# Kernel tuning notes

Hardware: AMD Instinct MI355X
Metric: run time of the kernel (lower is better)

## Reference

```python
import jax, jax.numpy as jnp
import numpy as np

H = 1024   # hidden_size
V = 32000  # output_size (vocab)
B = 64     # batch
S = 2048   # encoder seq_len


def setup_inputs() -> dict:
    key = jax.random.key(0)
    ks = jax.random.split(key, 12)
    sc = 0.02
    return {
        "input_seq": jax.random.randint(ks[0], (B,), 0, V),
        "last_hidden": jax.random.normal(ks[1], (1, B, H), jnp.float32),
        "encoder_outputs": jax.random.normal(ks[2], (S, B, H), jnp.float32),
        "emb": jax.random.normal(ks[3], (V, H), jnp.float32) * sc,
        "w_ih": jax.random.normal(ks[4], (3 * H, H), jnp.float32) * sc,
        "w_hh": jax.random.normal(ks[5], (3 * H, H), jnp.float32) * sc,
        "b_ih": jnp.zeros((3 * H,), jnp.float32),
        "b_hh": jnp.zeros((3 * H,), jnp.float32),
        "attn_w": jax.random.normal(ks[6], (H, H), jnp.float32) * sc,
        "attn_b": jnp.zeros((H,), jnp.float32),
        "concat_w": jax.random.normal(ks[7], (H, 2 * H), jnp.float32) * sc,
        "concat_b": jnp.zeros((H,), jnp.float32),
        "out_w": jax.random.normal(ks[8], (V, H), jnp.float32) * sc,
        "out_b": jnp.zeros((V,), jnp.float32),
    }


def _forward(input_seq, last_hidden, encoder_outputs, emb, w_ih, w_hh, b_ih, b_hh,
             attn_w, attn_b, concat_w, concat_b, out_w, out_b):
    # 1. embedding (dropout = identity in eval)
    x = emb[input_seq]                      # [b, h]
    h = last_hidden[0]                      # [b, h]
    # 2. single-step GRU (PyTorch gate order: reset, update, new)
    gx = x @ w_ih.T + b_ih                  # [b, 3h]
    gh = h @ w_hh.T + b_hh                  # [b, 3h]
    r = jax.nn.sigmoid(gx[:, :H] + gh[:, :H])
    z = jax.nn.sigmoid(gx[:, H:2 * H] + gh[:, H:2 * H])
    n = jnp.tanh(gx[:, 2 * H:] + r * gh[:, 2 * H:])
    h_new = (1.0 - z) * n + z * h           # [b, h] = rnn_output
    # 3. Luong 'general' attention: score = y . (W enc + b)
    proj = jnp.einsum('sbh,gh->sbg', encoder_outputs, attn_w) + attn_b  # [s,b,h]
    scores = jnp.einsum('bh,sbh->bs', h_new, proj)                      # [b,s]
    attn_weights = jax.nn.softmax(scores, axis=-1)                      # [b,s]
    # 4. context = weights bmm encoder_outputs
    context = jnp.einsum('bs,sbh->bh', attn_weights, encoder_outputs)   # [b,h]
    # 5. concat -> linear -> tanh -> out
    cat = jnp.concatenate([h_new, context], axis=-1)                    # [b,2h]
    concat_output = jnp.tanh(cat @ concat_w.T + concat_b)               # [b,h]
    output = concat_output @ out_w.T + out_b                            # [b,V]
    return output, h_new[None], attn_weights[:, None, :]


def reference(input_seq, last_hidden, encoder_outputs, emb, w_ih, w_hh, b_ih, b_hh,
              attn_w, attn_b, concat_w, concat_b, out_w, out_b):
    return _forward(input_seq, last_hidden, encoder_outputs, emb, w_ih, w_hh, b_ih,
                    b_hh, attn_w, attn_b, concat_w, concat_b, out_w, out_b)
```

## Files before the change

### kernel.cpp

```cpp
#include <hip/hip_runtime.h>

#define HS 1024
#define VS 32000
#define BS 64
#define SS 2048
#define NCH 128
#define SCH (SS/NCH)

typedef __attribute__((ext_vector_type(4))) float f4v;
typedef __attribute__((ext_vector_type(8))) short s8v;

__device__ __forceinline__ float sigmf(float x) { return 1.0f / (1.0f + __expf(-x)); }

__device__ __forceinline__ short bf16c(float f) {
  unsigned u = __builtin_bit_cast(unsigned, f);
  u = (u + 0x7FFFu + ((u >> 16) & 1u)) >> 16;
  return (short)u;
}

__global__ __launch_bounds__(256) void k_prep(const int* __restrict__ idx,
    const float* __restrict__ emb, const float* __restrict__ hid,
    const float* __restrict__ aw, float* __restrict__ ht,
    short* __restrict__ fx, short* __restrict__ fh, short* __restrict__ awf) {
  int t = blockIdx.x * 256 + threadIdx.x;
  {
    int lane = t & 63, nt = (t >> 6) & 63, kt = t >> 12;
    int kr = kt * 32 + ((lane >> 4) & 3) * 8;
    int col = nt * 16 + (lane & 15);
    const float* sp = aw + (size_t)kr * HS + col;
    s8v v;
#pragma unroll
    for (int j = 0; j < 8; j++) v[j] = bf16c(sp[(size_t)j * HS]);
    *(s8v*)(awf + (size_t)t * 8) = v;
  }
  if (t < 65536) {
    int b = t >> 10, k = t & 1023;
    ht[k * BS + b] = hid[(size_t)b * HS + k];
  }
  if (t < 8192) {
    int lane = t & 63, ct = (t >> 6) & 3, kt = t >> 8;
    int col = ct * 16 + (lane & 15);
    int kr = kt * 32 + ((lane >> 4) & 3) * 8;
    const float* sp = emb + (size_t)idx[col] * HS + kr;
    s8v v;
#pragma unroll
    for (int j = 0; j < 8; j++) v[j] = bf16c(sp[j]);
    *(s8v*)(fx + (size_t)t * 8) = v;
  } else if (t < 16384) {
    int t2 = t - 8192;
    int lane = t2 & 63, ct = (t2 >> 6) & 3, kt = t2 >> 8;
    int col = ct * 16 + (lane & 15);
    int kr = kt * 32 + ((lane >> 4) & 3) * 8;
    const float* sp = hid + (size_t)col * HS + kr;
    s8v v;
#pragma unroll
    for (int j = 0; j < 8; j++) v[j] = bf16c(sp[j]);
    *(s8v*)(fh + (size_t)t2 * 8) = v;
  }
}

template<int K, int OL>
__global__ __launch_bounds__(256) void mfsk(
    const float* __restrict__ W0, const short* __restrict__ xf0,
    const float* __restrict__ bias0, void* __restrict__ dst0,
    const float* __restrict__ W1, const short* __restrict__ xf1,
    const float* __restrict__ bias1, void* __restrict__ dst1) {
  const float* W    = blockIdx.y ? W1 : W0;
  const short* xf   = blockIdx.y ? xf1 : xf0;
  const float* bias = blockIdx.y ? bias1 : bias0;
  void* dst         = blockIdx.y ? dst1 : dst0;
  int lane = threadIdx.x & 63;
  int ks = threadIdx.x >> 6;
  int mt = blockIdx.x;
  int row = mt * 16 + (lane & 15);
  const int KW = (K / 32) / 4;
  const float* wp = W + (size_t)row * K + ((lane >> 4) * 8);
  const s8v* xp = (const s8v*)xf + lane;
  f4v acc0 = {0,0,0,0}, acc1 = {0,0,0,0}, acc2 = {0,0,0,0}, acc3 = {0,0,0,0};
#pragma unroll 4
  for (int kk = 0; kk < KW; kk++) {
    int kt = ks * KW + kk;
    float4 wa = *(const float4*)(wp + (size_t)kt * 32);
    float4 wb = *(const float4*)(wp + (size_t)kt * 32 + 4);
    s8v a;
    a[0] = bf16c(wa.x); a[1] = bf16c(wa.y); a[2] = bf16c(wa.z); a[3] = bf16c(wa.w);
    a[4] = bf16c(wb.x); a[5] = bf16c(wb.y); a[6] = bf16c(wb.z); a[7] = bf16c(wb.w);
    const s8v* xk = xp + (size_t)kt * 256;
    acc0 = __builtin_amdgcn_mfma_f32_16x16x32_bf16(a, xk[0],   acc0, 0, 0, 0);
    acc1 = __builtin_amdgcn_mfma_f32_16x16x32_bf16(a, xk[64],  acc1, 0, 0, 0);
    acc2 = __builtin_amdgcn_mfma_f32_16x16x32_bf16(a, xk[128], acc2, 0, 0, 0);
    acc3 = __builtin_amdgcn_mfma_f32_16x16x32_bf16(a, xk[192], acc3, 0, 0, 0);
  }
  __shared__ float red[4][4][4][64];
#pragma unroll
  for (int r = 0; r < 4; r++) {
    red[ks][0][r][lane] = acc0[r];
    red[ks][1][r][lane] = acc1[r];
    red[ks][2][r][lane] = acc2[r];
    red[ks][3][r][lane] = acc3[r];
  }
  __syncthreads();
  int ct = ks;
  int rr0 = mt * 16 + (lane >> 4) * 4;
  int col = ct * 16 + (lane & 15);
#pragma unroll
  for (int r = 0; r < 4; r++) {
    float v = red[0][ct][r][lane] + red[1][ct][r][lane] +
              red[2][ct][r][lane] + red[3][ct][r][lane] + bias[rr0 + r];
    if (OL == 0)
      ((float*)dst)[(size_t)(rr0 + r) * BS + col] = v;
    else
      ((short*)dst)[(size_t)col * HS + rr0 + r] = bf16c(tanhf(v));
  }
}

__global__ __launch_bounds__(256) void k_hnew(const float* __restrict__ gxt,
    const float* __restrict__ ght, const float* __restrict__ ht,
    float* __restrict__ out_h, short* __restrict__ fcat) {
  int tid = blockIdx.x * 256 + threadIdx.x;
  int b = tid & 63, i = tid >> 6;
  float r = sigmf(gxt[i * BS + b] + ght[i * BS + b]);
  float z = sigmf(gxt[(HS + i) * BS + b] + ght[(HS + i) * BS + b]);
  float n = tanhf(gxt[(2 * HS + i) * BS + b] + r * ght[(2 * HS + i) * BS + b]);
  float hn = (1.0f - z) * n + z * ht[i * BS + b];
  out_h[(size_t)b * HS + i] = hn;
  int kt = i >> 5, j = i & 7;
  int lane = (b & 15) | (((i >> 3) & 3) << 4);
  int ct = b >> 4;
  fcat[((size_t)((kt * 4 + ct) * 64 + lane)) * 8 + j] = bf16c(hn);
}

__global__ __launch_bounds__(256) void k_qgemm(const float* __restrict__ hnr,
    const short* __restrict__ awf, float* __restrict__ qrow) {
  int lane = threadIdx.x & 63;
  int mt = threadIdx.x >> 6;
  int nt = blockIdx.x;
  const float* ap = hnr + (size_t)(mt * 16 + (lane & 15)) * HS + ((lane >> 4) * 8);
  const s8v* bp = (const s8v*)awf + (size_t)nt * 64 + lane;
  f4v acc = {0,0,0,0};
#pragma unroll 4
  for (int kt = 0; kt < 32; kt++) {
    float4 wa = *(const float4*)(ap + kt * 32);
    float4 wb = *(const float4*)(ap + kt * 32 + 4);
    s8v a;
    a[0] = bf16c(wa.x); a[1] = bf16c(wa.y); a[2] = bf16c(wa.z); a[3] = bf16c(wa.w);
    a[4] = bf16c(wb.x); a[5] = bf16c(wb.y); a[6] = bf16c(wb.z); a[7] = bf16c(wb.w);
    acc = __builtin_amdgcn_mfma_f32_16x16x32_bf16(a, bp[(size_t)kt * 4096], acc, 0, 0, 0);
  }
  int r0 = mt * 16 + (lane >> 4) * 4;
  int hcol = nt * 16 + (lane & 15);
#pragma unroll
  for (int r = 0; r < 4; r++)
    qrow[(size_t)(r0 + r) * HS + hcol] = acc[r];
}

__global__ __launch_bounds__(256) void k_attn(const float* __restrict__ enc,
    const float* __restrict__ qrow, float* __restrict__ scores,
    float* __restrict__ mch, float* __restrict__ lch, float* __restrict__ ctxp) {
  int lane = threadIdx.x & 63;
  int w = blockIdx.x * 4 + (threadIdx.x >> 6);
  int b = w & 63;
  int ch = w >> 6;
  const float* qb = qrow + (size_t)b * HS + lane * 4;
  float4 q0 = *(const float4*)(qb + 0);
  float4 q1 = *(const float4*)(qb + 256);
  float4 q2 = *(const float4*)(qb + 512);
  float4 q3 = *(const float4*)(qb + 768);
  int s0 = ch * SCH;
  const size_t sstr = (size_t)BS * HS;
  const float* ep = enc + ((size_t)s0 * BS + b) * HS + lane * 4;
  float4 eb[2][8];
#pragma unroll
  for (int u = 0; u < 2; u++) {
    eb[0][u * 4 + 0] = *(const float4*)(ep + u * sstr + 0);
    eb[0][u * 4 + 1] = *(const float4*)(ep + u * sstr + 256);
    eb[0][u * 4 + 2] = *(const float4*)(ep + u * sstr + 512);
    eb[0][u * 4 + 3] = *(const float4*)(ep + u * sstr + 768);
  }
  float m = -1e30f, l = 0.f;
  float4 a0 = {0,0,0,0}, a1 = {0,0,0,0}, a2 = {0,0,0,0}, a3 = {0,0,0,0};
#pragma unroll
  for (int it = 0; it < SCH / 2; it++) {
    const int cur = it & 1, nxt = cur ^ 1;
    if (it + 1 < SCH / 2) {
      const float* np = ep + (size_t)(2 * it + 2) * sstr;
#pragma unroll
      for (int u = 0; u < 2; u++) {
        eb[nxt][u * 4 + 0] = *(const float4*)(np + u * sstr + 0);
        eb[nxt][u * 4 + 1] = *(const float4*)(np + u * sstr + 256);
        eb[nxt][u * 4 + 2] = *(const float4*)(np + u * sstr + 512);
        eb[nxt][u * 4 + 3] = *(const float4*)(np + u * sstr + 768);
      }
    }
    float4 c0 = eb[cur][0], c1 = eb[cur][1], c2 = eb[cur][2], c3 = eb[cur][3];
    float4 c4 = eb[cur][4], c5 = eb[cur][5], c6 = eb[cur][6], c7 = eb[cur][7];
    float d0 = fmaf(c0.x,q0.x, fmaf(c0.y,q0.y, fmaf(c0.z,q0.z, c0.w*q0.w)));
    float d1 = fmaf(c1.x,q1.x, fmaf(c1.y,q1.y, fmaf(c1.z,q1.z, c1.w*q1.w)));
    float d2 = fmaf(c2.x,q2.x, fmaf(c2.y,q2.y, fmaf(c2.z,q2.z, c2.w*q2.w)));
    float d3 = fmaf(c3.x,q3.x, fmaf(c3.y,q3.y, fmaf(c3.z,q3.z, c3.w*q3.w)));
    float pa = (d0 + d1) + (d2 + d3);
    float e0 = fmaf(c4.x,q0.x, fmaf(c4.y,q0.y, fmaf(c4.z,q0.z, c4.w*q0.w)));
    float e1 = fmaf(c5.x,q1.x, fmaf(c5.y,q1.y, fmaf(c5.z,q1.z, c5.w*q1.w)));
    float e2 = fmaf(c6.x,q2.x, fmaf(c6.y,q2.y, fmaf(c6.z,q2.z, c6.w*q2.w)));
    float e3 = fmaf(c7.x,q3.x, fmaf(c7.y,q3.y, fmaf(c7.z,q3.z, c7.w*q3.w)));
    float pb = (e0 + e1) + (e2 + e3);
#pragma unroll
    for (int off = 32; off; off >>= 1) {
      pa += __shfl_xor(pa, off, 64);
      pb += __shfl_xor(pb, off, 64);
    }
    if (lane == 0) {
      scores[(size_t)b * SS + s0 + 2 * it]     = pa;
      scores[(size_t)b * SS + s0 + 2 * it + 1] = pb;
    }
    float mn = fmaxf(m, fmaxf(pa, pb));
    float sc  = __expf(m - mn);
    float pra = __expf(pa - mn);
    float prb = __expf(pb - mn);
    l = fmaf(l, sc, pra + prb);
    a0.x = fmaf(a0.x, sc, fmaf(pra, c0.x, prb * c4.x));
    a0.y = fmaf(a0.y, sc, fmaf(pra, c0.y, prb * c4.y));
    a0.z = fmaf(a0.z, sc, fmaf(pra, c0.z, prb * c4.z));
    a0.w = fmaf(a0.w, sc, fmaf(pra, c0.w, prb * c4.w));
    a1.x = fmaf(a1.x, sc, fmaf(pra, c1.x, prb * c5.x));
    a1.y = fmaf(a1.y, sc, fmaf(pra, c1.y, prb * c5.y));
    a1.z = fmaf(a1.z, sc, fmaf(pra, c1.z, prb * c5.z));
    a1.w = fmaf(a1.w, sc, fmaf(pra, c1.w, prb * c5.w));
    a2.x = fmaf(a2.x, sc, fmaf(pra, c2.x, prb * c6.x));
    a2.y = fmaf(a2.y, sc, fmaf(pra, c2.y, prb * c6.y));
    a2.z = fmaf(a2.z, sc, fmaf(pra, c2.z, prb * c6.z));
    a2.w = fmaf(a2.w, sc, fmaf(pra, c2.w, prb * c6.w));
    a3.x = fmaf(a3.x, sc, fmaf(pra, c3.x, prb * c7.x));
    a3.y = fmaf(a3.y, sc, fmaf(pra, c3.y, prb * c7.y));
    a3.z = fmaf(a3.z, sc, fmaf(pra, c3.z, prb * c7.z));
    a3.w = fmaf(a3.w, sc, fmaf(pra, c3.w, prb * c7.w));
    m = mn;
  }
  if (lane == 0) { mch[b * NCH + ch] = m; lch[b * NCH + ch] = l; }
  float* cp = ctxp + ((size_t)(b * NCH + ch)) * HS + lane * 4;
  *(float4*)(cp + 0)   = a0;
  *(float4*)(cp + 256) = a1;
  *(float4*)(cp + 512) = a2;
  *(float4*)(cp + 768) = a3;
}

__global__ __launch_bounds__(256) void k_combine(const float* __restrict__ mch,
    const float* __restrict__ lch, const float* __restrict__ ctxp,
    const float* __restrict__ scores, short* __restrict__ fcat,
    float* __restrict__ wout) {
  int b = blockIdx.x;
  int t = threadIdx.x;
  __shared__ float sm[NCH], sl[NCH], ssc[NCH];
  if (t < NCH) { sm[t] = mch[b * NCH + t]; sl[t] = lch[b * NCH + t]; }
  __syncthreads();
  float mstar = -1e30f;
  for (int c = 0; c < NCH; c++) mstar = fmaxf(mstar, sm[c]);
  if (t < NCH) ssc[t] = __expf(sm[t] - mstar);
  __syncthreads();
  float L = 0.f;
  for (int c = 0; c < NCH; c++) L = fmaf(sl[c], ssc[c], L);
  float invL = 1.0f / L;
  int h = blockIdx.y * 256 + t;
  float acc = 0.f;
  for (int c = 0; c < NCH; c++)
    acc = fmaf(ctxp[((size_t)(b * NCH + c)) * HS + h], ssc[c], acc);
  float ctx = acc * invL;
  int kc = HS + h;
  int kt = kc >> 5, j = kc & 7;
  int lane2 = (b & 15) | (((kc >> 3) & 3) << 4);
  int ct = b >> 4;
  fcat[((size_t)((kt * 4 + ct) * 64 + lane2)) * 8 + j] = bf16c(ctx);
  if (blockIdx.y == 0)
    for (int s = t; s < SS; s += 256)
      wout[(size_t)b * SS + s] = __expf(scores[(size_t)b * SS + s] - mstar) * invL;
}

__global__ __launch_bounds__(256) void k_out2(const short* __restrict__ cbf,
    const float* __restrict__ ow, const float* __restrict__ ob,
    float* __restrict__ out0) {
  int lane = threadIdx.x & 63;
  int wv = threadIdx.x >> 6;
  int nt = blockIdx.x * 4 + wv;
  int v0 = nt * 16;
  const float* wp = ow + (size_t)(v0 + (lane & 15)) * HS + ((lane >> 4) * 8);
  const short* a0p = cbf + (size_t)(0  + (lane & 15)) * HS + ((lane >> 4) * 8);
  const short* a1p = a0p + (size_t)16 * HS;
  const short* a2p = a0p + (size_t)32 * HS;
  const short* a3p = a0p + (size_t)48 * HS;
  f4v acc0 = {0,0,0,0}, acc1 = {0,0,0,0}, acc2 = {0,0,0,0}, acc3 = {0,0,0,0};
#pragma unroll 2
  for (int kt = 0; kt < 32; kt++) {
    float4 wa = *(const float4*)(wp + kt * 32);
    float4 wb = *(const float4*)(wp + kt * 32 + 4);
    s8v bf;
    bf[0] = bf16c(wa.x); bf[1] = bf16c(wa.y); bf[2] = bf16c(wa.z); bf[3] = bf16c(wa.w);
    bf[4] = bf16c(wb.x); bf[5] = bf16c(wb.y); bf[6] = bf16c(wb.z); bf[7] = bf16c(wb.w);
    s8v fa0 = *(const s8v*)(a0p + kt * 32);
    s8v fa1 = *(const s8v*)(a1p + kt * 32);
    s8v fa2 = *(const s8v*)(a2p + kt * 32);
    s8v fa3 = *(const s8v*)(a3p + kt * 32);
    acc0 = __builtin_amdgcn_mfma_f32_16x16x32_bf16(fa0, bf, acc0, 0, 0, 0);
    acc1 = __builtin_amdgcn_mfma_f32_16x16x32_bf16(fa1, bf, acc1, 0, 0, 0);
    acc2 = __builtin_amdgcn_mfma_f32_16x16x32_bf16(fa2, bf, acc2, 0, 0, 0);
    acc3 = __builtin_amdgcn_mfma_f32_16x16x32_bf16(fa3, bf, acc3, 0, 0, 0);
  }
  float bv = ob[v0 + (lane & 15)];
  int rb = (lane >> 4) * 4;
  int vc = v0 + (lane & 15);
#pragma unroll
  for (int r = 0; r < 4; r++) {
    out0[(size_t)(0  + rb + r) * VS + vc] = acc0[r] + bv;
    out0[(size_t)(16 + rb + r) * VS + vc] = acc1[r] + bv;
    out0[(size_t)(32 + rb + r) * VS + vc] = acc2[r] + bv;
    out0[(size_t)(48 + rb + r) * VS + vc] = acc3[r] + bv;
  }
}

extern "C" void kernel_launch(void* const* d_in, const int* in_sizes, int n_in,
                              void* d_out, int out_size, void* d_ws, size_t ws_size,
                              hipStream_t stream) {
  const int*   idx  = (const int*)d_in[0];
  const float* hid  = (const float*)d_in[1];
  const float* enc  = (const float*)d_in[2];
  const float* emb  = (const float*)d_in[3];
  const float* w_ih = (const float*)d_in[4];
  const float* w_hh = (const float*)d_in[5];
  const float* b_ih = (const float*)d_in[6];
  const float* b_hh = (const float*)d_in[7];
  const float* aw   = (const float*)d_in[8];
  const float* cw   = (const float*)d_in[10];
  const float* cb   = (const float*)d_in[11];
  const float* ow   = (const float*)d_in[12];
  const float* ob   = (const float*)d_in[13];

  float* out0  = (float*)d_out;
  float* out_h = out0 + (size_t)BS * VS;
  float* out_w = out_h + (size_t)BS * HS;

  float* ws   = (float*)d_ws;
  float* gxt  = ws;
  float* ght  = gxt + (size_t)3 * HS * BS;
  float* ht   = ght + (size_t)3 * HS * BS;
  float* qrow = ht  + (size_t)HS * BS;
  float* scr  = qrow + (size_t)HS * BS;
  float* mch  = scr + (size_t)BS * SS;
  float* lch  = mch + (size_t)BS * NCH;
  float* ctxp = lch + (size_t)BS * NCH;
  short* awf  = (short*)(ctxp + (size_t)BS * NCH * HS);
  short* fx   = awf + (size_t)HS * HS;
  short* fh   = fx  + (size_t)HS * BS;
  short* fcat = fh  + (size_t)HS * BS;
  short* cbf  = fcat + (size_t)2 * HS * BS;

  k_prep   <<<dim3(512), dim3(256), 0, stream>>>(idx, emb, hid, aw, ht, fx, fh, awf);
  mfsk<HS, 0><<<dim3(3 * HS / 16, 2), dim3(256), 0, stream>>>(
      w_ih, fx, b_ih, gxt, w_hh, fh, b_hh, ght);
  k_hnew   <<<dim3(HS * BS / 256), dim3(256), 0, stream>>>(gxt, ght, ht, out_h, fcat);
  k_qgemm  <<<dim3(HS / 16), dim3(256), 0, stream>>>(out_h, awf, qrow);
  k_attn   <<<dim3(BS * NCH / 4), dim3(256), 0, stream>>>(enc, qrow, scr, mch, lch, ctxp);
  k_combine<<<dim3(BS, 4), dim3(256), 0, stream>>>(mch, lch, ctxp, scr, fcat, out_w);
  mfsk<2 * HS, 1><<<dim3(HS / 16, 1), dim3(256), 0, stream>>>(
      cw, fcat, cb, cbf, cw, fcat, cb, cbf);
  k_out2   <<<dim3(VS / 64), dim3(256), 0, stream>>>(cbf, ow, ob, out0);
}
```

Baseline: 255.3 us.

## Simplify attention streaming loop, halve chunk count, raise occupancy bound

Cuts the number of sequence chunks per batch row from 128 to 64, so each wave handles 32 positions. The fully unrolled two-row double-buffered loop becomes a rolled single-row loop that prefetches one row ahead, and k_attn gets a launch-bounds occupancy hint of 4. Together these lower register pressure so more waves can hide memory latency, and shrink the partial-context traffic into the combine step. The cost is less memory-level parallelism per wave and fewer blocks, which could leave bandwidth unused. The output GEMV loop unroll is also raised from 2 to 4.

```diff
diff --git a/kernel.cpp b/kernel.cpp
--- a/kernel.cpp
+++ b/kernel.cpp
@@ -4,7 +4,7 @@
 #define VS 32000
 #define BS 64
 #define SS 2048
-#define NCH 128
+#define NCH 64
 #define SCH (SS/NCH)
 
 typedef __attribute__((ext_vector_type(4))) float f4v;
@@ -154,7 +154,7 @@
     qrow[(size_t)(r0 + r) * HS + hcol] = acc[r];
 }
 
-__global__ __launch_bounds__(256) void k_attn(const float* __restrict__ enc,
+__global__ __launch_bounds__(256, 4) void k_attn(const float* __restrict__ enc,
     const float* __restrict__ qrow, float* __restrict__ scores,
     float* __restrict__ mch, float* __restrict__ lch, float* __restrict__ ctxp) {
   int lane = threadIdx.x & 63;
@@ -167,73 +167,43 @@
   float4 q2 = *(const float4*)(qb + 512);
   float4 q3 = *(const float4*)(qb + 768);
   int s0 = ch * SCH;
-  const size_t sstr = (size_t)BS * HS;
   const float* ep = enc + ((size_t)s0 * BS + b) * HS + lane * 4;
-  float4 eb[2][8];
-#pragma unroll
-  for (int u = 0; u < 2; u++) {
-    eb[0][u * 4 + 0] = *(const float4*)(ep + u * sstr + 0);
-    eb[0][u * 4 + 1] = *(const float4*)(ep + u * sstr + 256);
-    eb[0][u * 4 + 2] = *(const float4*)(ep + u * sstr + 512);
-    eb[0][u * 4 + 3] = *(const float4*)(ep + u * sstr + 768);
-  }
+  float4 e0 = *(const float4*)(ep + 0);
+  float4 e1 = *(const float4*)(ep + 256);
+  float4 e2 = *(const float4*)(ep + 512);
+  float4 e3 = *(const float4*)(ep + 768);
   float m = -1e30f, l = 0.f;
   float4 a0 = {0,0,0,0}, a1 = {0,0,0,0}, a2 = {0,0,0,0}, a3 = {0,0,0,0};
-#pragma unroll
-  for (int it = 0; it < SCH / 2; it++) {
-    const int cur = it & 1, nxt = cur ^ 1;
-    if (it + 1 < SCH / 2) {
-      const float* np = ep + (size_t)(2 * it + 2) * sstr;
-#pragma unroll
-      for (int u = 0; u < 2; u++) {
-        eb[nxt][u * 4 + 0] = *(const float4*)(np + u * sstr + 0);
-        eb[nxt][u * 4 + 1] = *(const float4*)(np + u * sstr + 256);
-        eb[nxt][u * 4 + 2] = *(const float4*)(np + u * sstr + 512);
-        eb[nxt][u * 4 + 3] = *(const float4*)(np + u * sstr + 768);
-      }
+  for (int si = 0; si < SCH; si++) {
+    float4 c0 = e0, c1 = e1, c2 = e2, c3 = e3;
+    if (si + 1 < SCH) {
+      const float* np = ep + (size_t)BS * HS;
+      e0 = *(const float4*)(np + 0);
+      e1 = *(const float4*)(np + 256);
+      e2 = *(const float4*)(np + 512);
+      e3 = *(const float4*)(np + 768);
     }
-    float4 c0 = eb[cur][0], c1 = eb[cur][1], c2 = eb[cur][2], c3 = eb[cur][3];
-    float4 c4 = eb[cur][4], c5 = eb[cur][5], c6 = eb[cur][6], c7 = eb[cur][7];
+    ep += (size_t)BS * HS;
     float d0 = fmaf(c0.x,q0.x, fmaf(c0.y,q0.y, fmaf(c0.z,q0.z, c0.w*q0.w)));
     float d1 = fmaf(c1.x,q1.x, fmaf(c1.y,q1.y, fmaf(c1.z,q1.z, c1.w*q1.w)));
     float d2 = fmaf(c2.x,q2.x, fmaf(c2.y,q2.y, fmaf(c2.z,q2.z, c2.w*q2.w)));
     float d3 = fmaf(c3.x,q3.x, fmaf(c3.y,q3.y, fmaf(c3.z,q3.z, c3.w*q3.w)));
-    float pa = (d0 + d1) + (d2 + d3);
-    float e0 = fmaf(c4.x,q0.x, fmaf(c4.y,q0.y, fmaf(c4.z,q0.z, c4.w*q0.w)));
-    float e1 = fmaf(c5.x,q1.x, fmaf(c5.y,q1.y, fmaf(c5.z,q1.z, c5.w*q1.w)));
-    float e2 = fmaf(c6.x,q2.x, fmaf(c6.y,q2.y, fmaf(c6.z,q2.z, c6.w*q2.w)));
-    float e3 = fmaf(c7.x,q3.x, fmaf(c7.y,q3.y, fmaf(c7.z,q3.z, c7.w*q3.w)));
-    float pb = (e0 + e1) + (e2 + e3);
-#pragma unroll
-    for (int off = 32; off; off >>= 1) {
-      pa += __shfl_xor(pa, off, 64);
-      pb += __shfl_xor(pb, off, 64);
-    }
-    if (lane == 0) {
-      scores[(size_t)b * SS + s0 + 2 * it]     = pa;
-      scores[(size_t)b * SS + s0 + 2 * it + 1] = pb;
-    }
-    float mn = fmaxf(m, fmaxf(pa, pb));
-    float sc  = __expf(m - mn);
-    float pra = __expf(pa - mn);
-    float prb = __expf(pb - mn);
-    l = fmaf(l, sc, pra + prb);
-    a0.x = fmaf(a0.x, sc, fmaf(pra, c0.x, prb * c4.x));
-    a0.y = fmaf(a0.y, sc, fmaf(pra, c0.y, prb * c4.y));
-    a0.z = fmaf(a0.z, sc, fmaf(pra, c0.z, prb * c4.z));
-    a0.w = fmaf(a0.w, sc, fmaf(pra, c0.w, prb * c4.w));
-    a1.x = fmaf(a1.x, sc, fmaf(pra, c1.x, prb * c5.x));
-    a1.y = fmaf(a1.y, sc, fmaf(pra, c1.y, prb * c5.y));
-    a1.z = fmaf(a1.z, sc, fmaf(pra, c1.z, prb * c5.z));
-    a1.w = fmaf(a1.w, sc, fmaf(pra, c1.w, prb * c5.w));
-    a2.x = fmaf(a2.x, sc, fmaf(pra, c2.x, prb * c6.x));
-    a2.y = fmaf(a2.y, sc, fmaf(pra, c2.y, prb * c6.y));
-    a2.z = fmaf(a2.z, sc, fmaf(pra, c2.z, prb * c6.z));
-    a2.w = fmaf(a2.w, sc, fmaf(pra, c2.w, prb * c6.w));
-    a3.x = fmaf(a3.x, sc, fmaf(pra, c3.x, prb * c7.x));
-    a3.y = fmaf(a3.y, sc, fmaf(pra, c3.y, prb * c7.y));
-    a3.z = fmaf(a3.z, sc, fmaf(pra, c3.z, prb * c7.z));
-    a3.w = fmaf(a3.w, sc, fmaf(pra, c3.w, prb * c7.w));
+    float p = (d0 + d1) + (d2 + d3);
+#pragma unroll
+    for (int off = 32; off; off >>= 1) p += __shfl_xor(p, off, 64);
+    if (lane == 0) scores[(size_t)b * SS + s0 + si] = p;
+    float mn = fmaxf(m, p);
+    float sc = __expf(m - mn);
+    float pr = __expf(p - mn);
+    l = fmaf(l, sc, pr);
+    a0.x = fmaf(a0.x, sc, pr * c0.x); a0.y = fmaf(a0.y, sc, pr * c0.y);
+    a0.z = fmaf(a0.z, sc, pr * c0.z); a0.w = fmaf(a0.w, sc, pr * c0.w);
+    a1.x = fmaf(a1.x, sc, pr * c1.x); a1.y = fmaf(a1.y, sc, pr * c1.y);
+    a1.z = fmaf(a1.z, sc, pr * c1.z); a1.w = fmaf(a1.w, sc, pr * c1.w);
+    a2.x = fmaf(a2.x, sc, pr * c2.x); a2.y = fmaf(a2.y, sc, pr * c2.y);
+    a2.z = fmaf(a2.z, sc, pr * c2.z); a2.w = fmaf(a2.w, sc, pr * c2.w);
+    a3.x = fmaf(a3.x, sc, pr * c3.x); a3.y = fmaf(a3.y, sc, pr * c3.y);
+    a3.z = fmaf(a3.z, sc, pr * c3.z); a3.w = fmaf(a3.w, sc, pr * c3.w);
     m = mn;
   }
   if (lane == 0) { mch[b * NCH + ch] = m; lch[b * NCH + ch] = l; }
@@ -288,7 +258,7 @@
   const short* a2p = a0p + (size_t)32 * HS;
   const short* a3p = a0p + (size_t)48 * HS;
   f4v acc0 = {0,0,0,0}, acc1 = {0,0,0,0}, acc2 = {0,0,0,0}, acc3 = {0,0,0,0};
-#pragma unroll 2
+#pragma unroll 4
   for (int kt = 0; kt < 32; kt++) {
     float4 wa = *(const float4*)(wp + kt * 32);
     float4 wb = *(const float4*)(wp + kt * 32 + 4);
```

Result: faster. 210.5 us (-17.5%).
